# Kernel optimization log

Measured on AMD Instinct MI355X. Metric: run time of the kernel, lower is better.

Reference implementation:

```python
import jax, jax.numpy as jnp
import numpy as np

D_MODEL = 1024
N_HEADS = 16
HEAD_DIM = D_MODEL // N_HEADS


def setup_inputs() -> dict:
    key = jax.random.key(0)
    k_x, k_wqkv, k_bqkv, k_wo, k_bo = jax.random.split(key, 5)
    b, t = 4, 2048
    s = 1.0 / np.sqrt(D_MODEL)
    return {
        "x": jax.random.normal(k_x, (b, t, D_MODEL), dtype=jnp.float32),
        "w_qkv": jax.random.uniform(k_wqkv, (D_MODEL, 3 * D_MODEL), jnp.float32, -s, s),
        "b_qkv": jax.random.uniform(k_bqkv, (3 * D_MODEL,), jnp.float32, -s, s),
        "w_out": jax.random.uniform(k_wo, (D_MODEL, D_MODEL), jnp.float32, -s, s),
        "b_out": jax.random.uniform(k_bo, (D_MODEL,), jnp.float32, -s, s),
    }


def reference(x, w_qkv, b_qkv, w_out, b_out):
    b, t, _ = x.shape
    # fused QKV projection -> [b, t, 3, h, d] -> q,k,v each [b, h, t, d]
    qkv = (x @ w_qkv + b_qkv).reshape(b, t, 3, N_HEADS, HEAD_DIM)
    q, k, v = jnp.moveaxis(qkv, 2, 0)          # each [b, t, h, d]
    q = q.transpose(0, 2, 1, 3)                # [b, h, t, d]
    k = k.transpose(0, 2, 1, 3)
    v = v.transpose(0, 2, 1, 3)
    scale = 1.0 / np.sqrt(HEAD_DIM).astype(np.float32)
    logits = jnp.einsum('bhqd,bhkd->bhqk', q, k) * scale
    causal = jnp.tril(jnp.ones((t, t), dtype=bool))
    logits = jnp.where(causal, logits, jnp.finfo(logits.dtype).min)
    attn = jax.nn.softmax(logits, axis=-1)
    out = jnp.einsum('bhqk,bhkd->bhqd', attn, v)      # [b, h, t, d]
    out = out.transpose(0, 2, 1, 3).reshape(b, t, D_MODEL)
    return out @ w_out + b_out
```

## Files before the change

kernel.cpp:

```cpp
#include <hip/hip_runtime.h>
#include <hip/hip_bf16.h>
#include <math.h>

#define NHEADS 16
#define HDIM   64
#define SEQT   2048
#define NBATCH 4
#define DMODEL 1024
#define MROWS  (NBATCH * SEQT)

typedef __bf16 bf16;
typedef bf16  bf16x8 __attribute__((ext_vector_type(8)));
typedef float f32x4  __attribute__((ext_vector_type(4)));

#define MFMA_BF16(a, b, c) __builtin_amdgcn_mfma_f32_16x16x32_bf16((a), (b), (c), 0, 0, 0)

__device__ __forceinline__ void gload_lds16(const void* g, void* l) {
  __builtin_amdgcn_global_load_lds((const __attribute__((address_space(1))) void*)g,
                                   (__attribute__((address_space(3))) void*)l, 16, 0, 0);
}


__global__ __launch_bounds__(256) void k_cvt_f32_bf16(const float* __restrict__ in,
                                                      bf16* __restrict__ out, int n8) {
  int i = blockIdx.x * blockDim.x + threadIdx.x;
  if (i >= n8) return;
  const float4* in4 = (const float4*)in;
  float4 a = in4[(size_t)i * 2], b = in4[(size_t)i * 2 + 1];
  bf16x8 v;
  v[0] = (bf16)a.x; v[1] = (bf16)a.y; v[2] = (bf16)a.z; v[3] = (bf16)a.w;
  v[4] = (bf16)b.x; v[5] = (bf16)b.y; v[6] = (bf16)b.z; v[7] = (bf16)b.w;
  *(bf16x8*)(out + (size_t)i * 8) = v;
}

__global__ __launch_bounds__(256) void k_transpose_f32_bf16(const float* __restrict__ in,
                                                            bf16* __restrict__ out,
                                                            int R, int C) {
  int nct = C >> 6;
  int rt = blockIdx.x / nct, ct = blockIdx.x % nct;
  __shared__ float tile[64][65];
  int tid = threadIdx.x;
#pragma unroll
  for (int i = 0; i < 16; i++) {
    int e = i * 256 + tid, r = e >> 6, c = e & 63;
    tile[r][c] = in[(size_t)(rt * 64 + r) * C + ct * 64 + c];
  }
  __syncthreads();
#pragma unroll
  for (int i = 0; i < 16; i++) {
    int e = i * 256 + tid, r = e >> 6, c = e & 63;
    out[(size_t)(ct * 64 + r) * R + rt * 64 + c] = (bf16)tile[c][r];
  }
}

__global__ __launch_bounds__(256) void k_transpose_v(const bf16* __restrict__ v,
                                                     bf16* __restrict__ vt) {
  int tt = blockIdx.x & 31;
  int bh = blockIdx.x >> 5;
  __shared__ bf16 tile[64][65];
  int tid = threadIdx.x;
  const bf16* src = v + (size_t)bh * SEQT * 64 + (size_t)tt * 64 * 64;
#pragma unroll
  for (int i = 0; i < 16; i++) {
    int e = i * 256 + tid, r = e >> 6, c = e & 63;
    tile[r][c] = src[r * 64 + c];
  }
  __syncthreads();
  bf16* dst = vt + (size_t)bh * 64 * SEQT + tt * 64;
#pragma unroll
  for (int i = 0; i < 16; i++) {
    int e = i * 256 + tid, r = e >> 6, c = e & 63;
    dst[(size_t)r * SEQT + c] = tile[c][r];
  }
}


__device__ __forceinline__ void gemm128_core(const bf16* __restrict__ A,
                                             const bf16* __restrict__ Bt,
                                             int K, int bm, int bn, char* smem,
                                             f32x4 (&acc)[4][4]) {
  int tid = threadIdx.x, lane = tid & 63, w = tid >> 6;
  int l15 = lane & 15, g = lane >> 4;
  int wrow = (w >> 1) * 64, wcol = (w & 1) * 64;
  char* As = smem;
  char* Bs = smem + 8192;
  const char* Ag = (const char*)(A + (size_t)bm * 128 * K);
  const char* Bg = (const char*)(Bt + (size_t)bn * 128 * K);
  const int rowB = K * 2;
  int srow = w * 16 + (lane >> 2);
  int scol = (lane & 3) * 16;

  for (int kt = 0; kt < K / 32; kt++) {
#pragma unroll
    for (int is = 0; is < 2; is++) {
      int row = is * 64 + srow;
      gload_lds16(Ag + (size_t)row * rowB + kt * 64 + scol, As + is * 4096 + w * 1024);
      gload_lds16(Bg + (size_t)row * rowB + kt * 64 + scol, Bs + is * 4096 + w * 1024);
    }
    __syncthreads();
    bf16x8 af[4], bfr[4];
#pragma unroll
    for (int i = 0; i < 4; i++)
      af[i] = *(const bf16x8*)&As[(wrow + i * 16 + l15) * 64 + g * 16];
#pragma unroll
    for (int j = 0; j < 4; j++)
      bfr[j] = *(const bf16x8*)&Bs[(wcol + j * 16 + l15) * 64 + g * 16];
#pragma unroll
    for (int i = 0; i < 4; i++)
#pragma unroll
      for (int j = 0; j < 4; j++)
        acc[i][j] = MFMA_BF16(af[i], bfr[j], acc[i][j]);
    __syncthreads();
  }
}

__global__ __launch_bounds__(256) void k_gemm_qkv(const bf16* __restrict__ A,
                                                  const bf16* __restrict__ Bt,
                                                  const float* __restrict__ bias,
                                                  bf16* __restrict__ Qo,
                                                  bf16* __restrict__ Ko,
                                                  bf16* __restrict__ Vo) {
  const int K = DMODEL, NB = 24;
  int bm = blockIdx.x / NB, bn = blockIdx.x % NB;
  __shared__ __align__(16) char smem[16384];
  f32x4 acc[4][4] = {};
  gemm128_core(A, Bt, K, bm, bn, smem, acc);

  int tid = threadIdx.x, lane = tid & 63, w = tid >> 6;
  int l15 = lane & 15, g = lane >> 4;
  int wrow = (w >> 1) * 64, wcol = (w & 1) * 64;
  int rowbase = bm * 128 + wrow;
  int b = (bm * 128) >> 11;
#pragma unroll
  for (int j = 0; j < 4; j++) {
    int n = bn * 128 + wcol + j * 16 + l15;
    float bj = bias[n];
    int which = n >> 10;
    int nn = n & 1023;
    int head = nn >> 6, d = nn & 63;
    bf16* dst = (which == 0) ? Qo : (which == 1) ? Ko : Vo;
    size_t base = ((size_t)(b * NHEADS + head) * SEQT) * 64 + d;
#pragma unroll
    for (int i = 0; i < 4; i++) {
#pragma unroll
      for (int r = 0; r < 4; r++) {
        int row = rowbase + i * 16 + g * 4 + r;
        int t = row & (SEQT - 1);
        dst[base + (size_t)t * 64] = (bf16)(acc[i][j][r] + bj);
      }
    }
  }
}

__global__ __launch_bounds__(256) void k_gemm_out(const bf16* __restrict__ A,
                                                  const bf16* __restrict__ Bt,
                                                  const float* __restrict__ bias,
                                                  float* __restrict__ C) {
  const int K = DMODEL, NB = 8;
  int bm = blockIdx.x / NB, bn = blockIdx.x % NB;
  __shared__ __align__(16) char smem[16384];
  f32x4 acc[4][4] = {};
  gemm128_core(A, Bt, K, bm, bn, smem, acc);

  int tid = threadIdx.x, lane = tid & 63, w = tid >> 6;
  int l15 = lane & 15, g = lane >> 4;
  int wrow = (w >> 1) * 64, wcol = (w & 1) * 64;
#pragma unroll
  for (int j = 0; j < 4; j++) {
    int n = bn * 128 + wcol + j * 16 + l15;
    float bj = bias[n];
#pragma unroll
    for (int i = 0; i < 4; i++) {
#pragma unroll
      for (int r = 0; r < 4; r++) {
        int row = bm * 128 + wrow + i * 16 + g * 4 + r;
        C[(size_t)row * DMODEL + n] = acc[i][j][r] + bj;
      }
    }
  }
}


__global__ __launch_bounds__(256) void k_attn(const bf16* __restrict__ Q,
                                              const bf16* __restrict__ Kg,
                                              const bf16* __restrict__ VT,
                                              bf16* __restrict__ Oo) {
  int bh = blockIdx.x & 63;
  int qi = blockIdx.x >> 6;
  int tid = threadIdx.x, lane = tid & 63, w = tid >> 6;
  int l15 = lane & 15, g = lane >> 4;
  __shared__ __align__(16) char smem[24576];
  char* Ks = smem;
  char* Vs = smem + 8192;
  char* Ps = smem + 16384 + w * 2048;

  const bf16* Qbh = Q  + (size_t)bh * SEQT * 64;
  const bf16* Kbh = Kg + (size_t)bh * SEQT * 64;
  const bf16* Vbh = VT + (size_t)bh * 64 * SEQT;
  int qlo = qi * 64 + w * 16;

  bf16x8 aq[2];
#pragma unroll
  for (int ks = 0; ks < 2; ks++) {
    bf16x8 v = *(const bf16x8*)(Qbh + (size_t)(qlo + l15) * 64 + ks * 32 + g * 8);
#pragma unroll
    for (int e = 0; e < 8; e++) v[e] = (bf16)((float)v[e] * 0.125f);
    aq[ks] = v;
  }

  float m[4], lsum[4];
  f32x4 o[4];
#pragma unroll
  for (int r = 0; r < 4; r++) { m[r] = -INFINITY; lsum[r] = 0.f; }
#pragma unroll
  for (int jd = 0; jd < 4; jd++) o[jd] = (f32x4){0.f, 0.f, 0.f, 0.f};

  for (int j = 0; j <= qi; j++) {
#pragma unroll
    for (int is = 0; is < 2; is++) {
      int p = is * 4096 + w * 1024 + (lane & 63) * 16;
      int row = p >> 7;
      int lg = p ^ ((row & 7) << 4);
      gload_lds16((const char*)(Kbh + (size_t)j * 4096) + lg,
                  Ks + is * 4096 + w * 1024);
      int cb = lg & 127;
      gload_lds16((const char*)(Vbh + (size_t)row * SEQT + j * 64) + cb,
                  Vs + is * 4096 + w * 1024);
    }
    __syncthreads();

    f32x4 s[4];
#pragma unroll
    for (int c = 0; c < 4; c++) {
      int row = c * 16 + l15;
      f32x4 t = {0.f, 0.f, 0.f, 0.f};
      t = MFMA_BF16(aq[0], *(const bf16x8*)&Ks[(row * 128 + 0  + g * 16) ^ ((l15 & 7) << 4)], t);
      t = MFMA_BF16(aq[1], *(const bf16x8*)&Ks[(row * 128 + 64 + g * 16) ^ ((l15 & 7) << 4)], t);
      s[c] = t;
    }

    bool diag = (j == qi);
    int qrb = w * 16 + g * 4;
#pragma unroll
    for (int r = 0; r < 4; r++) {
      float mx = -INFINITY;
#pragma unroll
      for (int c = 0; c < 4; c++) {
        float v = s[c][r];
        if (diag && (c * 16 + l15) > (qrb + r)) { v = -INFINITY; s[c][r] = v; }
        mx = fmaxf(mx, v);
      }
      mx = fmaxf(mx, __shfl_xor(mx, 1));
      mx = fmaxf(mx, __shfl_xor(mx, 2));
      mx = fmaxf(mx, __shfl_xor(mx, 4));
      mx = fmaxf(mx, __shfl_xor(mx, 8));
      float mn = fmaxf(m[r], mx);
      float co = __expf(m[r] - mn);
      m[r] = mn;
      float ssum = 0.f;
#pragma unroll
      for (int c = 0; c < 4; c++) {
        float p = __expf(s[c][r] - mn);
        s[c][r] = p;
        ssum += p;
      }
      ssum += __shfl_xor(ssum, 1);
      ssum += __shfl_xor(ssum, 2);
      ssum += __shfl_xor(ssum, 4);
      ssum += __shfl_xor(ssum, 8);
      lsum[r] = lsum[r] * co + ssum;
#pragma unroll
      for (int jd = 0; jd < 4; jd++) o[jd][r] *= co;
    }

#pragma unroll
    for (int c = 0; c < 4; c++) {
#pragma unroll
      for (int r = 0; r < 4; r++) {
        int row = g * 4 + r;
        int addr = (row * 128 + (c * 16 + l15) * 2) ^ ((row & 7) << 4);
        *(bf16*)&Ps[addr] = (bf16)s[c][r];
      }
    }

#pragma unroll
    for (int ks = 0; ks < 2; ks++) {
      bf16x8 pa = *(const bf16x8*)&Ps[(l15 * 128 + ks * 64 + g * 16) ^ ((l15 & 7) << 4)];
#pragma unroll
      for (int jd = 0; jd < 4; jd++) {
        int vrow = jd * 16 + l15;
        bf16x8 bv = *(const bf16x8*)&Vs[(vrow * 128 + ks * 64 + g * 16) ^ ((l15 & 7) << 4)];
        o[jd] = MFMA_BF16(pa, bv, o[jd]);
      }
    }
    __syncthreads();
  }

  int b = bh >> 4, h = bh & 15;
#pragma unroll
  for (int jd = 0; jd < 4; jd++) {
#pragma unroll
    for (int r = 0; r < 4; r++) {
      int t = qlo + g * 4 + r;
      float vv = o[jd][r] / lsum[r];
      Oo[((size_t)(b * SEQT + t)) * DMODEL + h * 64 + jd * 16 + l15] = (bf16)vv;
    }
  }
}


extern "C" void kernel_launch(void* const* d_in, const int* in_sizes, int n_in,
                              void* d_out, int out_size, void* d_ws, size_t ws_size,
                              hipStream_t stream) {
  const float* x     = (const float*)d_in[0];
  const float* w_qkv = (const float*)d_in[1];
  const float* b_qkv = (const float*)d_in[2];
  const float* w_out = (const float*)d_in[3];
  const float* b_out = (const float*)d_in[4];
  float* out = (float*)d_out;

  char* ws = (char*)d_ws;
  bf16* xb    = (bf16*)(ws);
  bf16* wqkvT = (bf16*)(ws + (16u << 20));
  bf16* woutT = (bf16*)(ws + (22u << 20));
  bf16* Qb    = (bf16*)(ws + (24u << 20));
  bf16* Kb    = (bf16*)(ws + (40u << 20));
  bf16* Vb    = (bf16*)(ws + (56u << 20));
  bf16* VTb   = (bf16*)(ws + (72u << 20));
  bf16* attn_o = xb;

  k_cvt_f32_bf16<<<(MROWS * DMODEL / 8 + 255) / 256, 256, 0, stream>>>(x, xb, MROWS * DMODEL / 8);
  k_transpose_f32_bf16<<<16 * 48, 256, 0, stream>>>(w_qkv, wqkvT, DMODEL, 3 * DMODEL);
  k_transpose_f32_bf16<<<16 * 16, 256, 0, stream>>>(w_out, woutT, DMODEL, DMODEL);
  k_gemm_qkv<<<64 * 24, 256, 0, stream>>>(xb, wqkvT, b_qkv, Qb, Kb, Vb);
  k_transpose_v<<<64 * 32, 256, 0, stream>>>(Vb, VTb);
  k_attn<<<32 * 64, 256, 0, stream>>>(Qb, Kb, VTb, attn_o);
  k_gemm_out<<<64 * 8, 256, 0, stream>>>(attn_o, woutT, b_out, out);
}
```

Before: 321.4 us.

## Double-buffer K/V tiles in attention, reverse block order, lazy softmax rescale

Attention now prefetches the next K/V tile into a second LDS buffer while computing on the current one, dropping the trailing barrier per iteration. Blocks are reversed so long causal rows start first for better load balance. The online-softmax rescaling of the accumulator is skipped unless a row max grows past a threshold, saving exps and multiplies. LDS use grows, which may reduce occupancy.

After: 306.8 us. 1.05x faster.

```diff
diff --git a/kernel.cpp b/kernel.cpp
--- a/kernel.cpp
+++ b/kernel.cpp
@@ -186,18 +186,23 @@
                                               const bf16* __restrict__ VT,
                                               bf16* __restrict__ Oo) {
   int bh = blockIdx.x & 63;
-  int qi = blockIdx.x >> 6;
+  int qi = 31 - (blockIdx.x >> 6);
   int tid = threadIdx.x, lane = tid & 63, w = tid >> 6;
   int l15 = lane & 15, g = lane >> 4;
-  __shared__ __align__(16) char smem[24576];
-  char* Ks = smem;
-  char* Vs = smem + 8192;
-  char* Ps = smem + 16384 + w * 2048;
+  __shared__ __align__(16) char smem[40960];
+  char* Ps = smem + 32768 + w * 2048;
 
   const bf16* Qbh = Q  + (size_t)bh * SEQT * 64;
-  const bf16* Kbh = Kg + (size_t)bh * SEQT * 64;
-  const bf16* Vbh = VT + (size_t)bh * 64 * SEQT;
+  const char* Kbyte = (const char*)(Kg + (size_t)bh * SEQT * 64);
+  const char* Vbyte = (const char*)(VT + (size_t)bh * 64 * SEQT);
   int qlo = qi * 64 + w * 16;
+
+  int pA = w * 1024 + lane * 16;
+  int pB = pA + 4096;
+  int rA = pA >> 7, rB = pB >> 7;
+  int lgA = pA ^ ((rA & 7) << 4), lgB = pB ^ ((rB & 7) << 4);
+  int vA = rA * 4096 + (lgA & 127), vB = rB * 4096 + (lgB & 127);
+  int dstA = w * 1024, dstB = 4096 + w * 1024;
 
   bf16x8 aq[2];
 #pragma unroll
@@ -215,19 +220,27 @@
 #pragma unroll
   for (int jd = 0; jd < 4; jd++) o[jd] = (f32x4){0.f, 0.f, 0.f, 0.f};
 
+  {
+    gload_lds16(Kbyte + lgA, smem + dstA);
+    gload_lds16(Kbyte + lgB, smem + dstB);
+    gload_lds16(Vbyte + vA, smem + 16384 + dstA);
+    gload_lds16(Vbyte + vB, smem + 16384 + dstB);
+  }
+
+  int cur = 0;
   for (int j = 0; j <= qi; j++) {
-#pragma unroll
-    for (int is = 0; is < 2; is++) {
-      int p = is * 4096 + w * 1024 + (lane & 63) * 16;
-      int row = p >> 7;
-      int lg = p ^ ((row & 7) << 4);
-      gload_lds16((const char*)(Kbh + (size_t)j * 4096) + lg,
-                  Ks + is * 4096 + w * 1024);
-      int cb = lg & 127;
-      gload_lds16((const char*)(Vbh + (size_t)row * SEQT + j * 64) + cb,
-                  Vs + is * 4096 + w * 1024);
-    }
     __syncthreads();
+    if (j < qi) {
+      int nx = cur ^ 1;
+      const char* kg = Kbyte + (size_t)(j + 1) * 8192;
+      const char* vg = Vbyte + (size_t)(j + 1) * 128;
+      gload_lds16(kg + lgA, smem + nx * 8192 + dstA);
+      gload_lds16(kg + lgB, smem + nx * 8192 + dstB);
+      gload_lds16(vg + vA, smem + 16384 + nx * 8192 + dstA);
+      gload_lds16(vg + vB, smem + 16384 + nx * 8192 + dstB);
+    }
+    char* Ks = smem + cur * 8192;
+    char* Vs = smem + 16384 + cur * 8192;
 
     f32x4 s[4];
 #pragma unroll
@@ -241,26 +254,43 @@
 
     bool diag = (j == qi);
     int qrb = w * 16 + g * 4;
+    float mx[4];
 #pragma unroll
     for (int r = 0; r < 4; r++) {
-      float mx = -INFINITY;
+      float v0 = -INFINITY;
 #pragma unroll
       for (int c = 0; c < 4; c++) {
         float v = s[c][r];
         if (diag && (c * 16 + l15) > (qrb + r)) { v = -INFINITY; s[c][r] = v; }
-        mx = fmaxf(mx, v);
-      }
-      mx = fmaxf(mx, __shfl_xor(mx, 1));
-      mx = fmaxf(mx, __shfl_xor(mx, 2));
-      mx = fmaxf(mx, __shfl_xor(mx, 4));
-      mx = fmaxf(mx, __shfl_xor(mx, 8));
-      float mn = fmaxf(m[r], mx);
-      float co = __expf(m[r] - mn);
-      m[r] = mn;
+        v0 = fmaxf(v0, v);
+      }
+      v0 = fmaxf(v0, __shfl_xor(v0, 1));
+      v0 = fmaxf(v0, __shfl_xor(v0, 2));
+      v0 = fmaxf(v0, __shfl_xor(v0, 4));
+      v0 = fmaxf(v0, __shfl_xor(v0, 8));
+      mx[r] = v0;
+    }
+
+    bool need = (mx[0] > m[0] + 8.f) | (mx[1] > m[1] + 8.f) |
+                (mx[2] > m[2] + 8.f) | (mx[3] > m[3] + 8.f);
+    if (__any(need)) {
+#pragma unroll
+      for (int r = 0; r < 4; r++) {
+        float mn = fmaxf(m[r], mx[r]);
+        float co = __expf(m[r] - mn);
+        m[r] = mn;
+        lsum[r] *= co;
+#pragma unroll
+        for (int jd = 0; jd < 4; jd++) o[jd][r] *= co;
+      }
+    }
+
+#pragma unroll
+    for (int r = 0; r < 4; r++) {
       float ssum = 0.f;
 #pragma unroll
       for (int c = 0; c < 4; c++) {
-        float p = __expf(s[c][r] - mn);
+        float p = __expf(s[c][r] - m[r]);
         s[c][r] = p;
         ssum += p;
       }
@@ -268,9 +298,7 @@
       ssum += __shfl_xor(ssum, 2);
       ssum += __shfl_xor(ssum, 4);
       ssum += __shfl_xor(ssum, 8);
-      lsum[r] = lsum[r] * co + ssum;
-#pragma unroll
-      for (int jd = 0; jd < 4; jd++) o[jd][r] *= co;
+      lsum[r] += ssum;
     }
 
 #pragma unroll
@@ -293,7 +321,7 @@
         o[jd] = MFMA_BF16(pa, bv, o[jd]);
       }
     }
-    __syncthreads();
+    cur ^= 1;
   }
 
   int b = bh >> 4, h = bh & 15;
```
